# Kernel tuning notes

Hardware: AMD Instinct MI355X
Metric: run time of the kernel (lower is better)

Reference implementation:

```python
import jax, jax.numpy as jnp
import numpy as np
from itertools import combinations

NUM_KERNELS = 84   # C(9,3) kernels: weight -1 everywhere, +2 at 3 positions
KLEN = 9
INDICES = np.array(list(combinations(range(KLEN), 3)), dtype=np.int32)  # (84, 3)

NUM_FEATURES = 9996          # 84 * 119
MAX_DILATIONS_PER_KERNEL = 32
N, L = 256, 1024


def _fit_dilations(input_length, num_features, max_dilations_per_kernel):
    # Deterministic replication of MiniRocket's _fit_dilations.
    nfpk = num_features // NUM_KERNELS
    true_max = min(nfpk, max_dilations_per_kernel)
    multiplier = nfpk / true_max
    max_exponent = np.log2((input_length - 1) / (KLEN - 1))
    dilations, counts = np.unique(
        np.logspace(0, max_exponent, true_max, base=2).astype(np.int32),
        return_counts=True,
    )
    nfpd = (counts * multiplier).astype(np.int32)
    remainder = nfpk - int(nfpd.sum())
    i = 0
    while remainder > 0:
        nfpd[i] += 1
        remainder -= 1
        i = (i + 1) % len(nfpd)
    return dilations, nfpd


def setup_inputs() -> dict:
    key = jax.random.key(0)
    k1, k2 = jax.random.split(key)
    x = jax.random.normal(k1, (N, 1, L), dtype=jnp.float32)
    biases = jax.random.normal(k2, (NUM_FEATURES,), dtype=jnp.float32)
    return {"x": x, "biases": biases}


def _transform(x2d, biases):
    # x2d: (N, L). MiniRocket algebraic trick: conv with weights in {-1, +2}
    n, length = x2d.shape
    dilations, nfpd = _fit_dilations(length, NUM_FEATURES, MAX_DILATIONS_PER_KERNEL)
    kernel_ids = np.arange(NUM_KERNELS)
    feats = []
    offset = 0
    for di, (d, f) in enumerate(zip(dilations.tolist(), nfpd.tolist())):
        p = ((KLEN - 1) * d) // 2  # 'same' padding = 4*d
        xp = jnp.pad(x2d, ((0, 0), (p, p)))
        # 9 dilated shifts, each (N, L)
        S = jnp.stack([xp[:, j * d: j * d + length] for j in range(KLEN)], axis=0)  # (9,N,L)
        C = 3.0 * S[INDICES].sum(axis=1) - S.sum(axis=0)[None]  # (84, N, L)
        b = biases[offset: offset + NUM_KERNELS * f].reshape(NUM_KERNELS, f)
        offset += NUM_KERNELS * f
        cmp = (C[:, None, :, :] > b[:, :, None, None]).astype(x2d.dtype)  # (84,f,N,L)
        ppv_full = cmp.mean(axis=-1)                      # padded kernels: whole series
        ppv_crop = cmp[..., p: length - p].mean(axis=-1)  # unpadded kernels: valid region
        padded = jnp.asarray(((di % 2) + kernel_ids) % 2 == 0)  # (84,)
        feat_d = jnp.where(padded[:, None, None], ppv_full, ppv_crop)  # (84, f, N)
        feats.append(feat_d.reshape(NUM_KERNELS * f, n))
    return jnp.concatenate(feats, axis=0).T  # (N, num_features)


def reference(x, biases):
    # x: (N, 1, L) univariate time series
    return _transform(x[:, 0, :], biases)
```

## Files before the change

### kernel.cpp

```cpp
#include <hip/hip_runtime.h>


namespace {

constexpr int LSER = 1024;
constexpr int NS   = 256;
constexpr int NFEAT = 9996;
constexpr int NDIL = 25;
constexpr int GK   = 6;
constexpr int TCH  = 64;
constexpr int NBLK = 7168;
constexpr int PADROWS = 2048;
constexpr int ROW0 = 512;

__constant__ int c_DIL[NDIL] = {1,2,3,4,5,6,7,8,10,12,14,16,19,22,26,31,36,42,50,58,68,79,93,109,127};
__constant__ int c_F[NDIL]   = {19,12,4,8,4,4,4,4,4,4,4,4,4,4,4,4,4,3,3,3,3,3,3,3,3};
__constant__ int c_FOFF[NDIL + 1] = {
    0,1596,2604,2940,3612,3948,4284,4620,4956,5292,5628,5964,6300,6636,6972,
    7308,7644,7980,8232,8484,8736,8988,9240,9492,9744,9996};
__constant__ int c_BSTART[NDIL + 1] = {
    0,1120,1792,2016,2464,2688,2912,3136,3360,3584,3808,4032,4256,4480,4704,
    4928,5152,5376,5600,5824,6048,6272,6496,6720,6944,7168};

constexpr int CIDX[84][3] = {
    {0,1,2},{0,1,3},{0,1,4},{0,1,5},{0,1,6},{0,1,7},{0,1,8},
    {0,2,3},{0,2,4},{0,2,5},{0,2,6},{0,2,7},{0,2,8},
    {0,3,4},{0,3,5},{0,3,6},{0,3,7},{0,3,8},
    {0,4,5},{0,4,6},{0,4,7},{0,4,8},
    {0,5,6},{0,5,7},{0,5,8},
    {0,6,7},{0,6,8},
    {0,7,8},
    {1,2,3},{1,2,4},{1,2,5},{1,2,6},{1,2,7},{1,2,8},
    {1,3,4},{1,3,5},{1,3,6},{1,3,7},{1,3,8},
    {1,4,5},{1,4,6},{1,4,7},{1,4,8},
    {1,5,6},{1,5,7},{1,5,8},
    {1,6,7},{1,6,8},
    {1,7,8},
    {2,3,4},{2,3,5},{2,3,6},{2,3,7},{2,3,8},
    {2,4,5},{2,4,6},{2,4,7},{2,4,8},
    {2,5,6},{2,5,7},{2,5,8},
    {2,6,7},{2,6,8},
    {2,7,8},
    {3,4,5},{3,4,6},{3,4,7},{3,4,8},
    {3,5,6},{3,5,7},{3,5,8},
    {3,6,7},{3,6,8},
    {3,7,8},
    {4,5,6},{4,5,7},{4,5,8},
    {4,6,7},{4,6,8},
    {4,7,8},
    {5,6,7},{5,6,8},
    {5,7,8},
    {6,7,8}};

__device__ __forceinline__ int imin(int a, int b) { return a < b ? a : b; }
__device__ __forceinline__ int imax(int a, int b) { return a > b ? a : b; }

template <int K0, int FS, int PSEL, int KK>
__device__ __forceinline__ void do_kernels(const float (&s)[9], float sum,
                                           const float (&bv)[GK][FS],
                                           unsigned (&cnt)[GK][FS]) {
  if constexpr (KK < GK) {
    if constexpr (PSEL < 0 || (((K0 + KK) & 1) == PSEL)) {
      constexpr int ia = CIDX[K0 + KK][0];
      constexpr int ib = CIDX[K0 + KK][1];
      constexpr int ic = CIDX[K0 + KK][2];
      float s3 = (s[ia] + s[ib]) + s[ic];
      float cv = __fsub_rn(__fmul_rn(3.0f, s3), sum);
#pragma unroll
      for (int j = 0; j < FS; ++j) cnt[KK][j] += (cv > bv[KK][j]) ? 1u : 0u;
    }
    do_kernels<K0, FS, PSEL, KK + 1>(s, sum, bv, cnt);
  }
}

template <int K0, int FS, int KK>
__device__ __forceinline__ void init_k(const float* __restrict__ biases,
                                       int colbase, int FTOT, int jb,
                                       float (&bv)[GK][FS], unsigned (&cnt)[GK][FS]) {
  if constexpr (KK < GK) {
    const int cb = colbase + (K0 + KK) * FTOT + jb;
#pragma unroll
    for (int j = 0; j < FS; ++j) {
      bv[KK][j] = biases[cb + j];
      cnt[KK][j] = 0u;
    }
    init_k<K0, FS, KK + 1>(biases, colbase, FTOT, jb, bv, cnt);
  }
}

template <int K0, int FS, int KK>
__device__ __forceinline__ void write_k(unsigned* __restrict__ outT, int colbase,
                                        int FTOT, int jb, int n,
                                        const unsigned (&cnt)[GK][FS]) {
  if constexpr (KK < GK) {
    const int cb = colbase + (K0 + KK) * FTOT + jb;
#pragma unroll
    for (int j = 0; j < FS; ++j) {
      atomicAdd(&outT[(cb + j) * NS + n], cnt[KK][j]);
    }
    write_k<K0, FS, KK + 1>(outT, colbase, FTOT, jb, n, cnt);
  }
}

template <int K0, int FS, int PSEL>
__device__ __forceinline__ void run_seg(int tlo, int thi, int d,
                                        const float* __restrict__ xb,
                                        const float (&bv)[GK][FS],
                                        unsigned (&cnt)[GK][FS]) {
#pragma unroll 1
  for (int t = tlo; t < thi; ++t) {
    float s[9];
#pragma unroll
    for (int j = 0; j < 9; ++j) s[j] = xb[(t + j * d) * NS];
    float sum = s[0];
#pragma unroll
    for (int j = 1; j < 9; ++j) sum += s[j];
    do_kernels<K0, FS, PSEL, 0>(s, sum, bv, cnt);
  }
}

template <int K0, int FS>
__device__ __forceinline__ void body(const float* __restrict__ xTp,
                                     const float* __restrict__ biases,
                                     unsigned* __restrict__ outT, int d, int par,
                                     int FTOT, int jb, int colbase, int ts) {
  const int n = (int)threadIdx.x;
  const float* xb = xTp + (ROW0 - 4 * d) * NS + n;

  float bv[GK][FS];
  unsigned cnt[GK][FS];
  init_k<K0, FS, 0>(biases, colbase, FTOT, jb, bv, cnt);

  const int p = 4 * d;
  const int t0 = ts * TCH, t1 = t0 + TCH;
  const int aHi = imin(t1, p);
  const int bLo = imax(t0, p), bHi = imin(t1, LSER - p);
  const int cLo = imax(t0, LSER - p);

  if (par == 0) {
    run_seg<K0, FS, 0>(t0, aHi, d, xb, bv, cnt);
  } else {
    run_seg<K0, FS, 1>(t0, aHi, d, xb, bv, cnt);
  }
  run_seg<K0, FS, -1>(bLo, bHi, d, xb, bv, cnt);
  if (par == 0) {
    run_seg<K0, FS, 0>(cLo, t1, d, xb, bv, cnt);
  } else {
    run_seg<K0, FS, 1>(cLo, t1, d, xb, bv, cnt);
  }

  write_k<K0, FS, 0>(outT, colbase, FTOT, jb, n, cnt);
}

template <int FS>
__device__ __forceinline__ void dispatch_g(int g, const float* __restrict__ xTp,
                                           const float* __restrict__ biases,
                                           unsigned* __restrict__ outT, int d, int par,
                                           int FTOT, int jb, int colbase, int ts) {
  switch (g) {
    case 0:  body<0,  FS>(xTp, biases, outT, d, par, FTOT, jb, colbase, ts); break;
    case 1:  body<6,  FS>(xTp, biases, outT, d, par, FTOT, jb, colbase, ts); break;
    case 2:  body<12, FS>(xTp, biases, outT, d, par, FTOT, jb, colbase, ts); break;
    case 3:  body<18, FS>(xTp, biases, outT, d, par, FTOT, jb, colbase, ts); break;
    case 4:  body<24, FS>(xTp, biases, outT, d, par, FTOT, jb, colbase, ts); break;
    case 5:  body<30, FS>(xTp, biases, outT, d, par, FTOT, jb, colbase, ts); break;
    case 6:  body<36, FS>(xTp, biases, outT, d, par, FTOT, jb, colbase, ts); break;
    case 7:  body<42, FS>(xTp, biases, outT, d, par, FTOT, jb, colbase, ts); break;
    case 8:  body<48, FS>(xTp, biases, outT, d, par, FTOT, jb, colbase, ts); break;
    case 9:  body<54, FS>(xTp, biases, outT, d, par, FTOT, jb, colbase, ts); break;
    case 10: body<60, FS>(xTp, biases, outT, d, par, FTOT, jb, colbase, ts); break;
    case 11: body<66, FS>(xTp, biases, outT, d, par, FTOT, jb, colbase, ts); break;
    case 12: body<72, FS>(xTp, biases, outT, d, par, FTOT, jb, colbase, ts); break;
    default: body<78, FS>(xTp, biases, outT, d, par, FTOT, jb, colbase, ts); break;
  }
}

}


__global__ __launch_bounds__(256) void mr_transpose(const float* __restrict__ x,
                                                    float* __restrict__ xTp) {
  __shared__ float tile[32][33];
  const int t0 = blockIdx.x << 5;
  const int n0 = blockIdx.y << 5;
  const int tx = threadIdx.x & 31, ty = threadIdx.x >> 5;
#pragma unroll
  for (int i = 0; i < 32; i += 8)
    tile[ty + i][tx] = x[(n0 + ty + i) * LSER + t0 + tx];
  __syncthreads();
#pragma unroll
  for (int i = 0; i < 32; i += 8)
    xTp[(ROW0 + t0 + ty + i) * NS + n0 + tx] = tile[tx][ty + i];
}

__global__ __launch_bounds__(256) void mr_main(const float* __restrict__ xTp,
                                               const float* __restrict__ biases,
                                               unsigned* __restrict__ outT) {
  const int bid = (int)blockIdx.x;
  int di = 0;
#pragma unroll 1
  while (di < NDIL - 1 && bid >= c_BSTART[di + 1]) ++di;
  const int rel = bid - c_BSTART[di];
  const int split = rel / 224;
  const int r2 = rel - split * 224;
  const int g = r2 >> 4;
  const int ts = r2 & 15;
  const int d = c_DIL[di];
  const int FTOT = c_F[di];
  const int colbase = c_FOFF[di];
  const int par = di & 1;
  const int jb = split << 2;
  const int FS = imin(4, FTOT - jb);

  if (FS == 4) {
    dispatch_g<4>(g, xTp, biases, outT, d, par, FTOT, jb, colbase, ts);
  } else {
    dispatch_g<3>(g, xTp, biases, outT, d, par, FTOT, jb, colbase, ts);
  }
}

__global__ __launch_bounds__(256) void mr_finalize(const unsigned* __restrict__ outT,
                                                   float* __restrict__ out) {
  __shared__ unsigned tile[64][65];
  __shared__ float sscale[64];
  const int tb = (int)blockIdx.x;
  const int ct = tb % 157, nt = tb / 157;
  const int c0 = ct << 6, n0 = nt << 6;
  const int tid = (int)threadIdx.x;

  if (tid < 64) {
    const int col = c0 + tid;
    float sc = 0.0f;
    if (col < NFEAT) {
      int di = 0;
      while (di < NDIL - 1 && col >= c_FOFF[di + 1]) ++di;
      const int rel = col - c_FOFF[di];
      const int f = c_F[di];
      const int k = rel / f;
      const int d = c_DIL[di];
      const bool padded = (((di + k) & 1) == 0);
      const int T = padded ? LSER : (LSER - 8 * d);
      sc = 1.0f / (float)T;
    }
    sscale[tid] = sc;
  }
#pragma unroll
  for (int i = 0; i < 16; ++i) {
    const int lin = tid + (i << 8);
    const int dc = lin >> 6, dn = lin & 63;
    const int col = c0 + dc;
    tile[dc][dn] = (col < NFEAT) ? outT[col * NS + n0 + dn] : 0u;
  }
  __syncthreads();
#pragma unroll
  for (int i = 0; i < 16; ++i) {
    const int lin = tid + (i << 8);
    const int dn = lin >> 6, dc = lin & 63;
    const int col = c0 + dc;
    if (col < NFEAT)
      out[(n0 + dn) * NFEAT + col] = (float)tile[dc][dn] * sscale[dc];
  }
}

extern "C" void kernel_launch(void* const* d_in, const int* in_sizes, int n_in,
                              void* d_out, int out_size, void* d_ws, size_t ws_size,
                              hipStream_t stream) {
  (void)in_sizes; (void)n_in; (void)out_size; (void)ws_size;
  const float* x = (const float*)d_in[0];
  const float* biases = (const float*)d_in[1];
  float* out = (float*)d_out;

  float* xTp = (float*)d_ws;
  unsigned* outT = (unsigned*)((char*)d_ws + (size_t)(PADROWS * NS * 4));

  hipMemsetAsync(d_ws, 0,
                 (size_t)PADROWS * NS * 4 + (size_t)NFEAT * NS * sizeof(unsigned),
                 stream);
  hipLaunchKernelGGL(mr_transpose, dim3(32, 8), dim3(256), 0, stream, x, xTp);
  hipLaunchKernelGGL(mr_main, dim3(NBLK), dim3(256), 0, stream, xTp, biases, outT);
  hipLaunchKernelGGL(mr_finalize, dim3(628), dim3(256), 0, stream, outT, out);
}
```

Baseline: 357.5 us.

## Process all biases per dilation in one block with per-dilation kernel grouping

Each block now handles every bias threshold for its dilation instead of splitting thresholds into chunks of four. The number of kernels per block (GK) is chosen per dilation so that GK*F stays around 48-57 counters. This cuts the block count roughly in half, so the 9-tap loads and the sum over taps are shared across more comparisons. The trade-offs are more registers per thread and larger per-dilation template instantiations, which raise code size.

```diff
diff --git a/kernel.cpp b/kernel.cpp
--- a/kernel.cpp
+++ b/kernel.cpp
@@ -7,9 +7,8 @@
 constexpr int NS   = 256;
 constexpr int NFEAT = 9996;
 constexpr int NDIL = 25;
-constexpr int GK   = 6;
 constexpr int TCH  = 64;
-constexpr int NBLK = 7168;
+constexpr int NBLK = 3472;
 constexpr int PADROWS = 2048;
 constexpr int ROW0 = 512;
 
@@ -19,8 +18,8 @@
     0,1596,2604,2940,3612,3948,4284,4620,4956,5292,5628,5964,6300,6636,6972,
     7308,7644,7980,8232,8484,8736,8988,9240,9492,9744,9996};
 __constant__ int c_BSTART[NDIL + 1] = {
-    0,1120,1792,2016,2464,2688,2912,3136,3360,3584,3808,4032,4256,4480,4704,
-    4928,5152,5376,5600,5824,6048,6272,6496,6720,6944,7168};
+    0,448,784,896,1120,1232,1344,1456,1568,1680,1792,1904,2016,2128,2240,
+    2352,2464,2576,2688,2800,2912,3024,3136,3248,3360,3472};
 
 constexpr int CIDX[84][3] = {
     {0,1,2},{0,1,3},{0,1,4},{0,1,5},{0,1,6},{0,1,7},{0,1,8},
@@ -55,7 +54,7 @@
 __device__ __forceinline__ int imin(int a, int b) { return a < b ? a : b; }
 __device__ __forceinline__ int imax(int a, int b) { return a > b ? a : b; }
 
-template <int K0, int FS, int PSEL, int KK>
+template <int GK, int K0, int FS, int PSEL, int KK>
 __device__ __forceinline__ void do_kernels(const float (&s)[9], float sum,
                                            const float (&bv)[GK][FS],
                                            unsigned (&cnt)[GK][FS]) {
@@ -69,40 +68,39 @@
 #pragma unroll
       for (int j = 0; j < FS; ++j) cnt[KK][j] += (cv > bv[KK][j]) ? 1u : 0u;
     }
-    do_kernels<K0, FS, PSEL, KK + 1>(s, sum, bv, cnt);
-  }
-}
-
-template <int K0, int FS, int KK>
+    do_kernels<GK, K0, FS, PSEL, KK + 1>(s, sum, bv, cnt);
+  }
+}
+
+template <int GK, int K0, int FS, int KK>
 __device__ __forceinline__ void init_k(const float* __restrict__ biases,
-                                       int colbase, int FTOT, int jb,
+                                       int colbase,
                                        float (&bv)[GK][FS], unsigned (&cnt)[GK][FS]) {
   if constexpr (KK < GK) {
-    const int cb = colbase + (K0 + KK) * FTOT + jb;
+    const int cb = colbase + (K0 + KK) * FS;
 #pragma unroll
     for (int j = 0; j < FS; ++j) {
       bv[KK][j] = biases[cb + j];
       cnt[KK][j] = 0u;
     }
-    init_k<K0, FS, KK + 1>(biases, colbase, FTOT, jb, bv, cnt);
-  }
-}
-
-template <int K0, int FS, int KK>
+    init_k<GK, K0, FS, KK + 1>(biases, colbase, bv, cnt);
+  }
+}
+
+template <int GK, int K0, int FS, int KK>
 __device__ __forceinline__ void write_k(unsigned* __restrict__ outT, int colbase,
-                                        int FTOT, int jb, int n,
-                                        const unsigned (&cnt)[GK][FS]) {
+                                        int n, const unsigned (&cnt)[GK][FS]) {
   if constexpr (KK < GK) {
-    const int cb = colbase + (K0 + KK) * FTOT + jb;
+    const int cb = colbase + (K0 + KK) * FS;
 #pragma unroll
     for (int j = 0; j < FS; ++j) {
       atomicAdd(&outT[(cb + j) * NS + n], cnt[KK][j]);
     }
-    write_k<K0, FS, KK + 1>(outT, colbase, FTOT, jb, n, cnt);
-  }
-}
-
-template <int K0, int FS, int PSEL>
+    write_k<GK, K0, FS, KK + 1>(outT, colbase, n, cnt);
+  }
+}
+
+template <int GK, int K0, int FS, int PSEL>
 __device__ __forceinline__ void run_seg(int tlo, int thi, int d,
                                         const float* __restrict__ xb,
                                         const float (&bv)[GK][FS],
@@ -115,21 +113,21 @@
     float sum = s[0];
 #pragma unroll
     for (int j = 1; j < 9; ++j) sum += s[j];
-    do_kernels<K0, FS, PSEL, 0>(s, sum, bv, cnt);
-  }
-}
-
-template <int K0, int FS>
+    do_kernels<GK, K0, FS, PSEL, 0>(s, sum, bv, cnt);
+  }
+}
+
+template <int GK, int K0, int FS>
 __device__ __forceinline__ void body(const float* __restrict__ xTp,
                                      const float* __restrict__ biases,
                                      unsigned* __restrict__ outT, int d, int par,
-                                     int FTOT, int jb, int colbase, int ts) {
+                                     int colbase, int ts) {
   const int n = (int)threadIdx.x;
   const float* xb = xTp + (ROW0 - 4 * d) * NS + n;
 
   float bv[GK][FS];
   unsigned cnt[GK][FS];
-  init_k<K0, FS, 0>(biases, colbase, FTOT, jb, bv, cnt);
+  init_k<GK, K0, FS, 0>(biases, colbase, bv, cnt);
 
   const int p = 4 * d;
   const int t0 = ts * TCH, t1 = t0 + TCH;
@@ -138,40 +136,31 @@
   const int cLo = imax(t0, LSER - p);
 
   if (par == 0) {
-    run_seg<K0, FS, 0>(t0, aHi, d, xb, bv, cnt);
+    run_seg<GK, K0, FS, 0>(t0, aHi, d, xb, bv, cnt);
   } else {
-    run_seg<K0, FS, 1>(t0, aHi, d, xb, bv, cnt);
-  }
-  run_seg<K0, FS, -1>(bLo, bHi, d, xb, bv, cnt);
+    run_seg<GK, K0, FS, 1>(t0, aHi, d, xb, bv, cnt);
+  }
+  run_seg<GK, K0, FS, -1>(bLo, bHi, d, xb, bv, cnt);
   if (par == 0) {
-    run_seg<K0, FS, 0>(cLo, t1, d, xb, bv, cnt);
+    run_seg<GK, K0, FS, 0>(cLo, t1, d, xb, bv, cnt);
   } else {
-    run_seg<K0, FS, 1>(cLo, t1, d, xb, bv, cnt);
-  }
-
-  write_k<K0, FS, 0>(outT, colbase, FTOT, jb, n, cnt);
-}
-
-template <int FS>
-__device__ __forceinline__ void dispatch_g(int g, const float* __restrict__ xTp,
-                                           const float* __restrict__ biases,
-                                           unsigned* __restrict__ outT, int d, int par,
-                                           int FTOT, int jb, int colbase, int ts) {
-  switch (g) {
-    case 0:  body<0,  FS>(xTp, biases, outT, d, par, FTOT, jb, colbase, ts); break;
-    case 1:  body<6,  FS>(xTp, biases, outT, d, par, FTOT, jb, colbase, ts); break;
-    case 2:  body<12, FS>(xTp, biases, outT, d, par, FTOT, jb, colbase, ts); break;
-    case 3:  body<18, FS>(xTp, biases, outT, d, par, FTOT, jb, colbase, ts); break;
-    case 4:  body<24, FS>(xTp, biases, outT, d, par, FTOT, jb, colbase, ts); break;
-    case 5:  body<30, FS>(xTp, biases, outT, d, par, FTOT, jb, colbase, ts); break;
-    case 6:  body<36, FS>(xTp, biases, outT, d, par, FTOT, jb, colbase, ts); break;
-    case 7:  body<42, FS>(xTp, biases, outT, d, par, FTOT, jb, colbase, ts); break;
-    case 8:  body<48, FS>(xTp, biases, outT, d, par, FTOT, jb, colbase, ts); break;
-    case 9:  body<54, FS>(xTp, biases, outT, d, par, FTOT, jb, colbase, ts); break;
-    case 10: body<60, FS>(xTp, biases, outT, d, par, FTOT, jb, colbase, ts); break;
-    case 11: body<66, FS>(xTp, biases, outT, d, par, FTOT, jb, colbase, ts); break;
-    case 12: body<72, FS>(xTp, biases, outT, d, par, FTOT, jb, colbase, ts); break;
-    default: body<78, FS>(xTp, biases, outT, d, par, FTOT, jb, colbase, ts); break;
+    run_seg<GK, K0, FS, 1>(cLo, t1, d, xb, bv, cnt);
+  }
+
+  write_k<GK, K0, FS, 0>(outT, colbase, n, cnt);
+}
+
+template <int GK, int FS, int G = 0>
+__device__ __forceinline__ void disp(int g, const float* __restrict__ xTp,
+                                     const float* __restrict__ biases,
+                                     unsigned* __restrict__ outT, int d, int par,
+                                     int colbase, int ts) {
+  if constexpr (G < 84 / GK) {
+    if (g == G) {
+      body<GK, G * GK, FS>(xTp, biases, outT, d, par, colbase, ts);
+    } else {
+      disp<GK, FS, G + 1>(g, xTp, biases, outT, d, par, colbase, ts);
+    }
   }
 }
 
@@ -201,21 +190,22 @@
 #pragma unroll 1
   while (di < NDIL - 1 && bid >= c_BSTART[di + 1]) ++di;
   const int rel = bid - c_BSTART[di];
-  const int split = rel / 224;
-  const int r2 = rel - split * 224;
-  const int g = r2 >> 4;
-  const int ts = r2 & 15;
+  const int g = rel >> 4;
+  const int ts = rel & 15;
   const int d = c_DIL[di];
-  const int FTOT = c_F[di];
   const int colbase = c_FOFF[di];
   const int par = di & 1;
-  const int jb = split << 2;
-  const int FS = imin(4, FTOT - jb);
-
-  if (FS == 4) {
-    dispatch_g<4>(g, xTp, biases, outT, d, par, FTOT, jb, colbase, ts);
+
+  if (di == 0) {
+    disp<3, 19>(g, xTp, biases, outT, d, par, colbase, ts);
+  } else if (di == 1) {
+    disp<4, 12>(g, xTp, biases, outT, d, par, colbase, ts);
+  } else if (di == 3) {
+    disp<6, 8>(g, xTp, biases, outT, d, par, colbase, ts);
+  } else if (di >= 17) {
+    disp<12, 3>(g, xTp, biases, outT, d, par, colbase, ts);
   } else {
-    dispatch_g<3>(g, xTp, biases, outT, d, par, FTOT, jb, colbase, ts);
+    disp<12, 4>(g, xTp, biases, outT, d, par, colbase, ts);
   }
 }
 
```

Result: slower. 396.0 us (+10.8%).
